# Performance work log

Measured on AMD Instinct MI355X. Metric: run time of the kernel, lower is better.

Reference implementation:

```python
import jax, jax.numpy as jnp
import numpy as np

EPS = 1e-5

def _cell(x, h, c, Wih, Whh, bih, bhh):
    # torch LSTMCell gate order: i, f, g, o
    gates = x @ Wih.T + bih + h @ Whh.T + bhh
    i, f, g, o = jnp.split(gates, 4, axis=-1)
    c = jax.nn.sigmoid(f) * c + jax.nn.sigmoid(i) * jnp.tanh(g)
    h = jax.nn.sigmoid(o) * jnp.tanh(c)
    return h, c

def _bn(x, gamma, beta):
    # training-mode BatchNorm1d: batch statistics over dim 0
    mu = jnp.mean(x, 0)
    var = jnp.var(x, 0)
    return gamma * (x - mu) * jax.lax.rsqrt(var + EPS) + beta

def setup_inputs():
    key = jax.random.key(0)
    ks = jax.random.split(key, 24)
    B, T, I = 1024, 256, 128
    H1, H2, H3 = 256, 256, 32
    w = lambda k, shape: jax.random.normal(k, shape, jnp.float32) * 0.05
    return {
        'x': jax.random.normal(ks[0], (B, T, I), jnp.float32),
        'Wih1': w(ks[1], (4 * H1, I)),  'Whh1': w(ks[2], (4 * H1, H1)),
        'bih1': w(ks[3], (4 * H1,)),    'bhh1': w(ks[4], (4 * H1,)),
        'g1': jnp.ones((H1,), jnp.float32), 'b1': jnp.zeros((H1,), jnp.float32),
        'Wih2': w(ks[5], (4 * H2, H1)), 'Whh2': w(ks[6], (4 * H2, H2)),
        'bih2': w(ks[7], (4 * H2,)),    'bhh2': w(ks[8], (4 * H2,)),
        'g2': jnp.ones((H2,), jnp.float32), 'b2': jnp.zeros((H2,), jnp.float32),
        'Wih3': w(ks[9], (4 * H3, H2)), 'Whh3': w(ks[10], (4 * H3, H3)),
        'bih3': w(ks[11], (4 * H3,)),   'bhh3': w(ks[12], (4 * H3,)),
        'g3': jnp.ones((H3,), jnp.float32), 'b3': jnp.zeros((H3,), jnp.float32),
        'Wl': w(ks[13], (2, H3)), 'bl': w(ks[14], (2,)),
        'Wl2': w(ks[15], (2, 2)), 'bl2': w(ks[16], (2,)),
    }

def reference(x, Wih1, Whh1, bih1, bhh1, g1, b1,
              Wih2, Whh2, bih2, bhh2, g2, b2,
              Wih3, Whh3, bih3, bhh3, g3, b3,
              Wl, bl, Wl2, bl2):
    B = x.shape[0]
    zeros = lambda d: jnp.zeros((B, d), x.dtype)
    carry0 = (zeros(256), zeros(256), zeros(256), zeros(256), zeros(32), zeros(32))

    def step(carry, xt):
        h1, c1, h2, c2, h3, c3 = carry
        h1, c1 = _cell(xt, h1, c1, Wih1, Whh1, bih1, bhh1)
        z = _bn(h1, g1, b1)
        h2, c2 = _cell(z, h2, c2, Wih2, Whh2, bih2, bhh2)
        z = _bn(h2, g2, b2)
        h3, c3 = _cell(z, h3, c3, Wih3, Whh3, bih3, bhh3)
        z = _bn(h3, g3, b3)
        z = jax.nn.relu(z @ Wl.T + bl)
        z = jax.nn.softmax(z @ Wl2.T + bl2, axis=-1)
        return (h1, c1, h2, c2, h3, c3), z

    _, ys = jax.lax.scan(step, carry0, jnp.swapaxes(x, 0, 1))  # ys: [T, B, 2]
    return jnp.swapaxes(ys, 0, 1)  # [B, T, 2]
```

## Files before the change

### kernel.cpp

```cpp
#include <hip/hip_runtime.h>
#include <hip/hip_cooperative_groups.h>

namespace cg = cooperative_groups;

#define B    1024
#define T    256
#define NBLK 256
#define NTHR 512
#define EPS  1e-5f

typedef _Float16 f16;
typedef _Float16 f16x8 __attribute__((ext_vector_type(8)));
typedef float    f32x4 __attribute__((ext_vector_type(4)));
typedef unsigned long long u64;

#define WS_H1X 0u
#define WS_H2X 1048576u
#define WS_H3X 2097152u
#define WS_ST  2228224u
#define WS_BAR 2297856u

#define OW1 0
#define OW2 25088
#define OW3 58368
#define OA1 67840
#define OD1 68864
#define OB1 69888
#define OB2 70016
#define OB3 70144
#define OA3 70160
#define OD3 70288
#define OHW 70416
#define OC1 70704
#define OC2 74928
#define OC3 79152
#define OA2 79680
#define OD2 80704
#define OG1 81728
#define OT1 82752
#define OG2 83776
#define OT2 84800
#define OG3 85824
#define OT3 85952
#define OR1 86080
#define OR2 86592
#define OR3 87104
#define LDSBYTES 87168

__device__ __forceinline__ float fsigmoid(float v) { return 1.f / (1.f + __expf(-v)); }
__device__ __forceinline__ float ftanh(float v)    { return 1.f - 2.f / (__expf(2.f * v) + 1.f); }

__device__ __forceinline__ float coh_ldf(const float* p) {
    return __hip_atomic_load(p, __ATOMIC_RELAXED, __HIP_MEMORY_SCOPE_AGENT);
}
__device__ __forceinline__ void coh_stf(float* p, float v) {
    __hip_atomic_store(p, v, __ATOMIC_RELAXED, __HIP_MEMORY_SCOPE_AGENT);
}

__device__ __forceinline__ void ld_phase(const float* sp, const f16* p1, const f16* p2,
                                         const f16* p3,
    f32x4& r0, f32x4& r1, f32x4& r2, f32x4& r3,
    f16x8& d0, f16x8& d1, f16x8& d2, f16x8& d3,
    f16x8& d4, f16x8& d5, f16x8& d6, f16x8& d7,
    f16x8& e0, f16x8& e1, f16x8& e2, f16x8& e3,
    f16x8& e4, f16x8& e5, f16x8& e6, f16x8& e7,
    f16x8& f0) {
    asm volatile(
        "global_load_dwordx4 %0, %21, off sc0 sc1\n\t"
        "global_load_dwordx4 %1, %21, off offset:16 sc0 sc1\n\t"
        "global_load_dwordx4 %2, %21, off offset:32 sc0 sc1\n\t"
        "global_load_dwordx4 %3, %21, off offset:48 sc0 sc1\n\t"
        "global_load_dwordx4 %4, %22, off sc0\n\t"
        "global_load_dwordx4 %5, %22, off offset:64 sc0\n\t"
        "global_load_dwordx4 %6, %22, off offset:128 sc0\n\t"
        "global_load_dwordx4 %7, %22, off offset:192 sc0\n\t"
        "global_load_dwordx4 %8, %22, off offset:256 sc0\n\t"
        "global_load_dwordx4 %9, %22, off offset:320 sc0\n\t"
        "global_load_dwordx4 %10, %22, off offset:384 sc0\n\t"
        "global_load_dwordx4 %11, %22, off offset:448 sc0\n\t"
        "global_load_dwordx4 %12, %23, off sc0\n\t"
        "global_load_dwordx4 %13, %23, off offset:64 sc0\n\t"
        "global_load_dwordx4 %14, %23, off offset:128 sc0\n\t"
        "global_load_dwordx4 %15, %23, off offset:192 sc0\n\t"
        "global_load_dwordx4 %16, %23, off offset:256 sc0\n\t"
        "global_load_dwordx4 %17, %23, off offset:320 sc0\n\t"
        "global_load_dwordx4 %18, %23, off offset:384 sc0\n\t"
        "global_load_dwordx4 %19, %23, off offset:448 sc0\n\t"
        "global_load_dwordx4 %20, %24, off sc0\n\t"
        "s_waitcnt vmcnt(0)"
        : "=&v"(r0), "=&v"(r1), "=&v"(r2), "=&v"(r3),
          "=&v"(d0), "=&v"(d1), "=&v"(d2), "=&v"(d3),
          "=&v"(d4), "=&v"(d5), "=&v"(d6), "=&v"(d7),
          "=&v"(e0), "=&v"(e1), "=&v"(e2), "=&v"(e3),
          "=&v"(e4), "=&v"(e5), "=&v"(e6), "=&v"(e7),
          "=&v"(f0)
        : "v"(sp), "v"(p1), "v"(p2), "v"(p3) : "memory");
}
__device__ __forceinline__ void ld_h4_sc0(const f16* p, f16x8& d0, f16x8& d1, f16x8& d2, f16x8& d3) {
    asm volatile(
        "global_load_dwordx4 %0, %4, off sc0\n\t"
        "global_load_dwordx4 %1, %4, off offset:16 sc0\n\t"
        "global_load_dwordx4 %2, %4, off offset:32 sc0\n\t"
        "global_load_dwordx4 %3, %4, off offset:48 sc0\n\t"
        "s_waitcnt vmcnt(0)"
        : "=&v"(d0), "=&v"(d1), "=&v"(d2), "=&v"(d3)
        : "v"(p) : "memory");
}
__device__ __forceinline__ void st_h2_sc0(f16* p, f16 v) {
    asm volatile("global_store_short %0, %1, off sc0" :: "v"(p), "v"(v) : "memory");
}

__global__ void __launch_bounds__(NTHR) cryptonet_kernel(
    const float* __restrict__ x,
    const float* __restrict__ Wih1, const float* __restrict__ Whh1,
    const float* __restrict__ bih1, const float* __restrict__ bhh1,
    const float* __restrict__ g1v,  const float* __restrict__ b1v,
    const float* __restrict__ Wih2, const float* __restrict__ Whh2,
    const float* __restrict__ bih2, const float* __restrict__ bhh2,
    const float* __restrict__ g2v,  const float* __restrict__ b2v,
    const float* __restrict__ Wih3, const float* __restrict__ Whh3,
    const float* __restrict__ bih3, const float* __restrict__ bhh3,
    const float* __restrict__ g3v,  const float* __restrict__ b3v,
    const float* __restrict__ Wl,   const float* __restrict__ bl,
    const float* __restrict__ Wl2,  const float* __restrict__ bl2,
    float* __restrict__ out, float* __restrict__ ws)
{
    cg::grid_group grid = cg::this_grid();
    const int tid  = threadIdx.x;
    const int blk  = blockIdx.x;
    const int CG   = blk >> 3;
    const int BGr  = blk & 7;
    const int b0   = BGr * 128;
    const int wv   = tid >> 6;
    const int lane = tid & 63;
    const int q    = lane >> 4;
    const int mlo  = lane & 15;

    extern __shared__ char smraw[];
    f16*   w1  = (f16*)(smraw + OW1);
    f16*   w2  = (f16*)(smraw + OW2);
    f16*   w3  = (f16*)(smraw + OW3);
    float* sA1 = (float*)(smraw + OA1);
    float* sD1 = (float*)(smraw + OD1);
    float* sA2 = (float*)(smraw + OA2);
    float* sD2 = (float*)(smraw + OD2);
    float* sB1 = (float*)(smraw + OB1);
    float* sB2 = (float*)(smraw + OB2);
    float* sB3 = (float*)(smraw + OB3);
    float* sA3 = (float*)(smraw + OA3);
    float* sD3 = (float*)(smraw + OD3);
    float* sHW = (float*)(smraw + OHW);
    float* c1  = (float*)(smraw + OC1);
    float* c2  = (float*)(smraw + OC2);
    float* c3  = (float*)(smraw + OC3);
    float* sG1 = (float*)(smraw + OG1);
    float* sT1 = (float*)(smraw + OT1);
    float* sG2 = (float*)(smraw + OG2);
    float* sT2 = (float*)(smraw + OT2);
    float* sG3 = (float*)(smraw + OG3);
    float* sT3 = (float*)(smraw + OT3);
    float* sR1 = (float*)(smraw + OR1);
    float* sR2 = (float*)(smraw + OR2);
    float* sR3 = (float*)(smraw + OR3);

    char* ws8 = (char*)ws;
    f16*   h1x   = (f16*)(ws8 + WS_H1X);
    f16*   h2x   = (f16*)(ws8 + WS_H2X);
    f16*   h3x   = (f16*)(ws8 + WS_H3X);
    float* stats = (float*)(ws8 + WS_ST);
    unsigned* bar = (unsigned*)(ws8 + WS_BAR);

    for (int idx = tid; idx < 32 * 384; idx += NTHR) {
        const int rr = idx / 384, k = idx - rr * 384;
        const int j = (rr >> 3) * 256 + CG * 8 + (rr & 7);
        const float v = (k < 128) ? Wih1[(size_t)j * 128 + k] : Whh1[(size_t)j * 256 + (k - 128)];
        w1[rr * 392 + k] = (f16)v;
    }
    for (int idx = tid; idx < 32 * 512; idx += NTHR) {
        const int rr = idx >> 9, k = idx & 511;
        const int j = (rr >> 3) * 256 + CG * 8 + (rr & 7);
        const float v = (k < 256) ? Wih2[(size_t)j * 256 + k] : Whh2[(size_t)j * 256 + (k - 256)];
        w2[rr * 520 + k] = (f16)v;
    }
    for (int idx = tid; idx < 16 * 296; idx += NTHR) w3[idx] = (f16)0.f;
    __syncthreads();
    for (int idx = tid; idx < 4 * 288; idx += NTHR) {
        const int rr = idx / 288, k = idx - rr * 288;
        const int j = rr * 32 + CG;
        const float v = (k < 256) ? Wih3[(size_t)j * 256 + k] : Whh3[(size_t)j * 32 + (k - 256)];
        w3[rr * 296 + k] = (f16)v;
    }
    if (tid < 32) {
        const int j = (tid >> 3) * 256 + CG * 8 + (tid & 7);
        sB1[tid] = bih1[j] + bhh1[j];
        sB2[tid] = bih2[j] + bhh2[j];
    }
    if (tid >= 32 && tid < 36) {
        const int g = tid - 32;
        sB3[g] = bih3[g * 32 + CG] + bhh3[g * 32 + CG];
    }
    if (tid >= 64 && tid < 136) {
        const int i = tid - 64;
        float v;
        if (i < 64) v = Wl[i];
        else if (i < 68) v = Wl2[i - 64];
        else if (i < 70) v = bl[i - 68];
        else v = bl2[i - 70];
        sHW[i] = v;
    }
    if (tid < 256) {
        sG1[tid] = g1v[tid]; sT1[tid] = b1v[tid];
        sG2[tid] = g2v[tid]; sT2[tid] = b2v[tid];
        if (tid < 32) { sG3[tid] = g3v[tid]; sT3[tid] = b3v[tid]; }
    }
    for (int i = tid; i < 8 * 132; i += NTHR) { c1[i] = 0.f; c2[i] = 0.f; }
    if (tid < 132) c3[tid] = 0.f;
    {
        unsigned int* z1 = (unsigned int*)h1x;
        unsigned int* z2 = (unsigned int*)h2x;
        unsigned int* z3 = (unsigned int*)h3x;
        const int gt = blk * NTHR + tid, gs = NBLK * NTHR;
        for (int i = gt; i < 131072; i += gs) z1[i] = 0u;
        for (int i = gt; i < 131072; i += gs) z2[i] = 0u;
        for (int i = gt; i < 16384;  i += gs) z3[i] = 0u;
        for (int i = gt; i < 256;    i += gs) bar[i] = 0u;
    }
    grid.sync();

    auto pointwise12 = [&](float* cst, f16* hdst, float* redp, const float* bias,
                           f32x4 acc0, f32x4 acc1) {
        float fr[4], orr[4];
        #pragma unroll
        for (int r = 0; r < 4; ++r) {
            fr[r]  = __shfl_xor(acc0[r], 8);
            orr[r] = __shfl_xor(acc1[r], 8);
        }
        float s = 0.f, sq = 0.f;
        const int c = mlo & 7;
        if (mlo < 8) {
            const float bi = bias[c], bf = bias[8 + c], bg = bias[16 + c], bo = bias[24 + c];
            float4 cc = *(float4*)&cst[c * 132 + wv * 16 + q * 4];
            float cv[4] = {cc.x, cc.y, cc.z, cc.w};
            #pragma unroll
            for (int r = 0; r < 4; ++r) {
                const float gi = fsigmoid(acc0[r] + bi);
                const float gf = fsigmoid(fr[r] + bf);
                const float gg = ftanh(acc1[r] + bg);
                const float go = fsigmoid(orr[r] + bo);
                const float cn = gf * cv[r] + gi * gg;
                cv[r] = cn;
                const f16 h16 = (f16)(go * ftanh(cn));
                st_h2_sc0(&hdst[(size_t)(b0 + wv * 16 + q * 4 + r) * 256 + CG * 8 + c], h16);
                const float hq = (float)h16;
                s += hq; sq += hq * hq;
            }
            *(float4*)&cst[c * 132 + wv * 16 + q * 4] = make_float4(cv[0], cv[1], cv[2], cv[3]);
        }
        s  += __shfl_xor(s, 16);  s  += __shfl_xor(s, 32);
        sq += __shfl_xor(sq, 16); sq += __shfl_xor(sq, 32);
        if (mlo < 8 && q == 0) {
            redp[wv * 16 + c * 2]     = s;
            redp[wv * 16 + c * 2 + 1] = sq;
        }
    };

    f16x8 xpre[4];
    auto loadx = [&](int t) {
        if (t < T) {
            const int brow = b0 + wv * 16 + mlo;
            #pragma unroll
            for (int kt = 0; kt < 4; ++kt) {
                const float* xp = x + ((size_t)brow * T + t) * 128 + kt * 32 + q * 8;
                const float4 u = *(const float4*)xp;
                const float4 v = *(const float4*)(xp + 4);
                f16x8 a;
                a[0] = (f16)u.x; a[1] = (f16)u.y; a[2] = (f16)u.z; a[3] = (f16)u.w;
                a[4] = (f16)v.x; a[5] = (f16)v.y; a[6] = (f16)v.z; a[7] = (f16)v.w;
                xpre[kt] = a;
            }
        }
    };
    loadx(0);

    auto fold8 = [&](f16x8 a, const float* sA, const float* sD, int k) -> f16x8 {
        const float4 aa0 = *(const float4*)&sA[k];
        const float4 aa1 = *(const float4*)&sA[k + 4];
        const float4 dd0 = *(const float4*)&sD[k];
        const float4 dd1 = *(const float4*)&sD[k + 4];
        a[0] = (f16)(aa0.x * (float)a[0] + dd0.x);
        a[1] = (f16)(aa0.y * (float)a[1] + dd0.y);
        a[2] = (f16)(aa0.z * (float)a[2] + dd0.z);
        a[3] = (f16)(aa0.w * (float)a[3] + dd0.w);
        a[4] = (f16)(aa1.x * (float)a[4] + dd1.x);
        a[5] = (f16)(aa1.y * (float)a[5] + dd1.y);
        a[6] = (f16)(aa1.z * (float)a[6] + dd1.z);
        a[7] = (f16)(aa1.w * (float)a[7] + dd1.w);
        return a;
    };

    for (int s = 0; s < T + 3; ++s) {
        const int t2 = s - 1, t3 = s - 2, th = s - 3;
        const int brow = b0 + wv * 16 + mlo;

        const float* sp = stats + (tid < 256
                ? ((size_t)((s & 1) ^ 1) * 8704 + (size_t)tid * 16)
                : ((size_t)(s & 1) * 8704 + 4096 + (size_t)(tid - 256) * 16));
        const f16* p1 = h1x + (size_t)(s & 1) * B * 256 + (size_t)brow * 256 + q * 8;
        const f16* p2 = h2x + (size_t)((s & 1) ^ 1) * B * 256 + (size_t)brow * 256 + q * 8;
        const f16* p3 = h3x + (size_t)(s & 1) * B * 32 + (size_t)brow * 32 + q * 8;
        f32x4 r0, r1, r2, r3;
        f16x8 hd[8], he[8], hf;
        ld_phase(sp, p1, p2, p3, r0, r1, r2, r3,
                 hd[0], hd[1], hd[2], hd[3], hd[4], hd[5], hd[6], hd[7],
                 he[0], he[1], he[2], he[3], he[4], he[5], he[6], he[7], hf);

        if (t2 >= 0 && t2 < T && tid < 256) {
            const float sv = r0[0] + r0[2] + r1[0] + r1[2] + r2[0] + r2[2] + r3[0] + r3[2];
            const float qv = r0[1] + r0[3] + r1[1] + r1[3] + r2[1] + r2[3] + r3[1] + r3[3];
            const float mu = sv * (1.f / B);
            const float var = qv * (1.f / B) - mu * mu;
            const float a = sG1[tid] * rsqrtf(var + EPS);
            sA1[tid] = a; sD1[tid] = sT1[tid] - mu * a;
        }
        if (t3 >= 0 && t3 < T && tid >= 256) {
            const int ch = tid - 256;
            const float sv = r0[0] + r0[2] + r1[0] + r1[2] + r2[0] + r2[2] + r3[0] + r3[2];
            const float qv = r0[1] + r0[3] + r1[1] + r1[3] + r2[1] + r2[3] + r3[1] + r3[3];
            const float mu = sv * (1.f / B);
            const float var = qv * (1.f / B) - mu * mu;
            const float a = sG2[ch] * rsqrtf(var + EPS);
            sA2[ch] = a; sD2[ch] = sT2[ch] - mu * a;
        }
        if (CG == 0 && th >= 0 && tid < 32) {
            const float* sp3 = stats + (size_t)(th & 1) * 8704 + 8192 + (size_t)tid * 16;
            float sv = 0.f, qv = 0.f;
            #pragma unroll
            for (int g = 0; g < 8; ++g) {
                sv += coh_ldf(sp3 + g * 2);
                qv += coh_ldf(sp3 + g * 2 + 1);
            }
            const float mu = sv * (1.f / B);
            const float var = qv * (1.f / B) - mu * mu;
            const float a = sG3[tid] * rsqrtf(var + EPS);
            sA3[tid] = a; sD3[tid] = sT3[tid] - mu * a;
        }

        if (s < T) {
            f16* h1c = h1x + (size_t)((s & 1) ^ 1) * B * 256;
            f32x4 acc0 = {0.f, 0.f, 0.f, 0.f}, acc1 = {0.f, 0.f, 0.f, 0.f};
            #pragma unroll
            for (int kt = 0; kt < 12; ++kt) {
                const f16x8 av = (kt < 4) ? xpre[kt] : hd[kt - 4];
                const f16x8 bf0 = *(const f16x8*)(w1 + mlo * 392 + kt * 32 + q * 8);
                const f16x8 bf1 = *(const f16x8*)(w1 + (16 + mlo) * 392 + kt * 32 + q * 8);
                acc0 = __builtin_amdgcn_mfma_f32_16x16x32_f16(av, bf0, acc0, 0, 0, 0);
                acc1 = __builtin_amdgcn_mfma_f32_16x16x32_f16(av, bf1, acc1, 0, 0, 0);
            }
            pointwise12(c1, h1c, sR1, sB1, acc0, acc1);
        }
        __syncthreads();

        if (t2 >= 0 && t2 < T) {
            f16* h2c = h2x + (size_t)(s & 1) * B * 256;
            f32x4 acc0 = {0.f, 0.f, 0.f, 0.f}, acc1 = {0.f, 0.f, 0.f, 0.f};
            #pragma unroll
            for (int kt = 0; kt < 16; ++kt) {
                const f16x8 av = (kt < 8) ? fold8(hd[kt], sA1, sD1, kt * 32 + q * 8)
                                          : he[kt - 8];
                const f16x8 bf0 = *(const f16x8*)(w2 + mlo * 520 + kt * 32 + q * 8);
                const f16x8 bf1 = *(const f16x8*)(w2 + (16 + mlo) * 520 + kt * 32 + q * 8);
                acc0 = __builtin_amdgcn_mfma_f32_16x16x32_f16(av, bf0, acc0, 0, 0, 0);
                acc1 = __builtin_amdgcn_mfma_f32_16x16x32_f16(av, bf1, acc1, 0, 0, 0);
            }
            pointwise12(c2, h2c, sR2, sB2, acc0, acc1);
        }

        if (t3 >= 0 && t3 < T) {
            f16* h3c = h3x + (size_t)((s & 1) ^ 1) * B * 32;
            f32x4 acc0 = {0.f, 0.f, 0.f, 0.f};
            #pragma unroll
            for (int kt = 0; kt < 9; ++kt) {
                const f16x8 av = (kt < 8) ? fold8(he[kt], sA2, sD2, kt * 32 + q * 8) : hf;
                const f16x8 bf0 = *(const f16x8*)(w3 + mlo * 296 + kt * 32 + q * 8);
                acc0 = __builtin_amdgcn_mfma_f32_16x16x32_f16(av, bf0, acc0, 0, 0, 0);
            }
            float gi[4], gf_[4], gg_[4], go_[4];
            #pragma unroll
            for (int r = 0; r < 4; ++r) {
                gi[r]  = __shfl(acc0[r], (lane & 48) + 0);
                gf_[r] = __shfl(acc0[r], (lane & 48) + 1);
                gg_[r] = __shfl(acc0[r], (lane & 48) + 2);
                go_[r] = __shfl(acc0[r], (lane & 48) + 3);
            }
            float s_ = 0.f, sq = 0.f;
            if (mlo == 0) {
                float4 cc = *(float4*)&c3[wv * 16 + q * 4];
                float cv[4] = {cc.x, cc.y, cc.z, cc.w};
                #pragma unroll
                for (int r = 0; r < 4; ++r) {
                    const float i_ = fsigmoid(gi[r] + sB3[0]);
                    const float f_ = fsigmoid(gf_[r] + sB3[1]);
                    const float g_ = ftanh(gg_[r] + sB3[2]);
                    const float o_ = fsigmoid(go_[r] + sB3[3]);
                    const float cn = f_ * cv[r] + i_ * g_;
                    cv[r] = cn;
                    const f16 h16 = (f16)(o_ * ftanh(cn));
                    st_h2_sc0(&h3c[(size_t)(b0 + wv * 16 + q * 4 + r) * 32 + CG], h16);
                    const float hq = (float)h16;
                    s_ += hq; sq += hq * hq;
                }
                *(float4*)&c3[wv * 16 + q * 4] = make_float4(cv[0], cv[1], cv[2], cv[3]);
            }
            s_ += __shfl_xor(s_, 16); s_ += __shfl_xor(s_, 32);
            sq += __shfl_xor(sq, 16); sq += __shfl_xor(sq, 32);
            if (lane == 0) { sR3[wv * 2] = s_; sR3[wv * 2 + 1] = sq; }
        }

        if (CG == 0 && th >= 0) {
            const f16* hp3 = h3x + (size_t)(s & 1) * B * 32;
            if (lane < 16) {
                const int b = b0 + wv * 16 + lane;
                const f16* hp = hp3 + (size_t)b * 32;
                f16x8 hv0, hv1, hv2, hv3;
                ld_h4_sc0(hp, hv0, hv1, hv2, hv3);
                float zz[32];
                #pragma unroll
                for (int k2 = 0; k2 < 8; ++k2) {
                    zz[k2]      = (float)hv0[k2];
                    zz[8 + k2]  = (float)hv1[k2];
                    zz[16 + k2] = (float)hv2[k2];
                    zz[24 + k2] = (float)hv3[k2];
                }
                float y0 = sHW[68], y1 = sHW[69];
                #pragma unroll
                for (int ch = 0; ch < 32; ++ch) {
                    const float z = sA3[ch] * zz[ch] + sD3[ch];
                    y0 += sHW[ch] * z; y1 += sHW[32 + ch] * z;
                }
                y0 = fmaxf(y0, 0.f); y1 = fmaxf(y1, 0.f);
                const float u0 = sHW[64] * y0 + sHW[65] * y1 + sHW[70];
                const float u1 = sHW[66] * y0 + sHW[67] * y1 + sHW[71];
                const float m = fmaxf(u0, u1);
                const float e0 = __expf(u0 - m), e1 = __expf(u1 - m);
                const float inv = 1.f / (e0 + e1);
                *(float2*)&out[((size_t)b * T + th) * 2] = make_float2(e0 * inv, e1 * inv);
            }
        }

        if (s < T + 2) {
            __syncthreads();
            if (s < T && tid < 16) {
                const int i = tid, ch = CG * 8 + (i >> 1), j = i & 1;
                float v = sR1[i];
                #pragma unroll
                for (int w = 1; w < 8; ++w) v += sR1[w * 16 + i];
                coh_stf(stats + (size_t)(s & 1) * 8704 + (size_t)ch * 16 + BGr * 2 + j, v);
            }
            if (t2 >= 0 && t2 < T && tid >= 16 && tid < 32) {
                const int i = tid - 16, ch = CG * 8 + (i >> 1), j = i & 1;
                float v = sR2[i];
                #pragma unroll
                for (int w = 1; w < 8; ++w) v += sR2[w * 16 + i];
                coh_stf(stats + (size_t)(t2 & 1) * 8704 + 4096 + (size_t)ch * 16 + BGr * 2 + j, v);
            }
            if (t3 >= 0 && t3 < T && tid >= 32 && tid < 34) {
                const int i = tid - 32;
                float v = sR3[i];
                #pragma unroll
                for (int w = 1; w < 8; ++w) v += sR3[w * 2 + i];
                coh_stf(stats + (size_t)(t3 & 1) * 8704 + 8192 + (size_t)CG * 16 + BGr * 2 + i, v);
            }
            __syncthreads();
            if (tid == 0)
                __hip_atomic_store(bar + blk, (unsigned)(s + 1),
                                   __ATOMIC_RELAXED, __HIP_MEMORY_SCOPE_AGENT);
            loadx(s + 1);
            if (wv == 0) {
                const unsigned tgt = (unsigned)(s + 1);
                u64* fl = (u64*)bar;
                for (;;) {
                    const u64 a = __hip_atomic_load(fl + lane,
                                    __ATOMIC_RELAXED, __HIP_MEMORY_SCOPE_AGENT);
                    const u64 b = __hip_atomic_load(fl + 64 + lane,
                                    __ATOMIC_RELAXED, __HIP_MEMORY_SCOPE_AGENT);
                    const bool ok = ((unsigned)a >= tgt) && ((unsigned)(a >> 32) >= tgt) &&
                                    ((unsigned)b >= tgt) && ((unsigned)(b >> 32) >= tgt);
                    if (__all(ok)) break;
                    __builtin_amdgcn_s_sleep(1);
                }
            }
            __syncthreads();
        }
    }
}

extern "C" void kernel_launch(void* const* d_in, const int* in_sizes, int n_in,
                              void* d_out, int out_size, void* d_ws, size_t ws_size,
                              hipStream_t stream) {
    const float* x    = (const float*)d_in[0];
    const float* Wih1 = (const float*)d_in[1];
    const float* Whh1 = (const float*)d_in[2];
    const float* bih1 = (const float*)d_in[3];
    const float* bhh1 = (const float*)d_in[4];
    const float* g1   = (const float*)d_in[5];
    const float* b1   = (const float*)d_in[6];
    const float* Wih2 = (const float*)d_in[7];
    const float* Whh2 = (const float*)d_in[8];
    const float* bih2 = (const float*)d_in[9];
    const float* bhh2 = (const float*)d_in[10];
    const float* g2   = (const float*)d_in[11];
    const float* b2   = (const float*)d_in[12];
    const float* Wih3 = (const float*)d_in[13];
    const float* Whh3 = (const float*)d_in[14];
    const float* bih3 = (const float*)d_in[15];
    const float* bhh3 = (const float*)d_in[16];
    const float* g3   = (const float*)d_in[17];
    const float* b3   = (const float*)d_in[18];
    const float* Wl   = (const float*)d_in[19];
    const float* bl   = (const float*)d_in[20];
    const float* Wl2  = (const float*)d_in[21];
    const float* bl2  = (const float*)d_in[22];
    float* out = (float*)d_out;
    float* ws  = (float*)d_ws;

    const int dyn_lds = LDSBYTES;
    hipFuncSetAttribute((const void*)cryptonet_kernel,
                        hipFuncAttributeMaxDynamicSharedMemorySize, dyn_lds);

    void* args[] = { &x, &Wih1, &Whh1, &bih1, &bhh1, &g1, &b1,
                     &Wih2, &Whh2, &bih2, &bhh2, &g2, &b2,
                     &Wih3, &Whh3, &bih3, &bhh3, &g3, &b3,
                     &Wl, &bl, &Wl2, &bl2, &out, &ws };
    hipLaunchCooperativeKernel((const void*)cryptonet_kernel, dim3(NBLK), dim3(NTHR),
                               args, dyn_lds, stream);
}
```

Measured before the change: 4.880 ms.

## Split grid barrier into group-local wait and deferred global wait overlapping layer-1

The end-of-step barrier now waits only on the 32 blocks of the same batch group, since layer-1 depends only on h1 rows from that group. The global all-block wait is moved to after the layer-1 MFMA and pointwise work of the next step, so layer-1 compute overlaps with slower blocks finishing. The h1 loads are split out of the combined phase load so they can be issued before the global wait. This relaxes synchronisation and risks a race if any cross-group data, such as BN stats, is consumed before the deferred global wait.

```diff
diff --git a/kernel.cpp b/kernel.cpp
--- a/kernel.cpp
+++ b/kernel.cpp
@@ -57,44 +57,47 @@
     __hip_atomic_store(p, v, __ATOMIC_RELAXED, __HIP_MEMORY_SCOPE_AGENT);
 }
 
-__device__ __forceinline__ void ld_phase(const float* sp, const f16* p1, const f16* p2,
-                                         const f16* p3,
+__device__ __forceinline__ void ld_h8_sc0(const f16* p, f16x8& d0, f16x8& d1, f16x8& d2,
+                                          f16x8& d3, f16x8& d4, f16x8& d5, f16x8& d6, f16x8& d7) {
+    asm volatile(
+        "global_load_dwordx4 %0, %8, off sc0\n\t"
+        "global_load_dwordx4 %1, %8, off offset:64 sc0\n\t"
+        "global_load_dwordx4 %2, %8, off offset:128 sc0\n\t"
+        "global_load_dwordx4 %3, %8, off offset:192 sc0\n\t"
+        "global_load_dwordx4 %4, %8, off offset:256 sc0\n\t"
+        "global_load_dwordx4 %5, %8, off offset:320 sc0\n\t"
+        "global_load_dwordx4 %6, %8, off offset:384 sc0\n\t"
+        "global_load_dwordx4 %7, %8, off offset:448 sc0\n\t"
+        "s_waitcnt vmcnt(0)"
+        : "=&v"(d0), "=&v"(d1), "=&v"(d2), "=&v"(d3),
+          "=&v"(d4), "=&v"(d5), "=&v"(d6), "=&v"(d7)
+        : "v"(p) : "memory");
+}
+__device__ __forceinline__ void ld_sh13(const float* sp, const f16* p2, const f16* p3,
     f32x4& r0, f32x4& r1, f32x4& r2, f32x4& r3,
-    f16x8& d0, f16x8& d1, f16x8& d2, f16x8& d3,
-    f16x8& d4, f16x8& d5, f16x8& d6, f16x8& d7,
     f16x8& e0, f16x8& e1, f16x8& e2, f16x8& e3,
     f16x8& e4, f16x8& e5, f16x8& e6, f16x8& e7,
     f16x8& f0) {
     asm volatile(
-        "global_load_dwordx4 %0, %21, off sc0 sc1\n\t"
-        "global_load_dwordx4 %1, %21, off offset:16 sc0 sc1\n\t"
-        "global_load_dwordx4 %2, %21, off offset:32 sc0 sc1\n\t"
-        "global_load_dwordx4 %3, %21, off offset:48 sc0 sc1\n\t"
-        "global_load_dwordx4 %4, %22, off sc0\n\t"
-        "global_load_dwordx4 %5, %22, off offset:64 sc0\n\t"
-        "global_load_dwordx4 %6, %22, off offset:128 sc0\n\t"
-        "global_load_dwordx4 %7, %22, off offset:192 sc0\n\t"
-        "global_load_dwordx4 %8, %22, off offset:256 sc0\n\t"
-        "global_load_dwordx4 %9, %22, off offset:320 sc0\n\t"
-        "global_load_dwordx4 %10, %22, off offset:384 sc0\n\t"
-        "global_load_dwordx4 %11, %22, off offset:448 sc0\n\t"
-        "global_load_dwordx4 %12, %23, off sc0\n\t"
-        "global_load_dwordx4 %13, %23, off offset:64 sc0\n\t"
-        "global_load_dwordx4 %14, %23, off offset:128 sc0\n\t"
-        "global_load_dwordx4 %15, %23, off offset:192 sc0\n\t"
-        "global_load_dwordx4 %16, %23, off offset:256 sc0\n\t"
-        "global_load_dwordx4 %17, %23, off offset:320 sc0\n\t"
-        "global_load_dwordx4 %18, %23, off offset:384 sc0\n\t"
-        "global_load_dwordx4 %19, %23, off offset:448 sc0\n\t"
-        "global_load_dwordx4 %20, %24, off sc0\n\t"
+        "global_load_dwordx4 %0, %13, off sc0 sc1\n\t"
+        "global_load_dwordx4 %1, %13, off offset:16 sc0 sc1\n\t"
+        "global_load_dwordx4 %2, %13, off offset:32 sc0 sc1\n\t"
+        "global_load_dwordx4 %3, %13, off offset:48 sc0 sc1\n\t"
+        "global_load_dwordx4 %4, %14, off sc0\n\t"
+        "global_load_dwordx4 %5, %14, off offset:64 sc0\n\t"
+        "global_load_dwordx4 %6, %14, off offset:128 sc0\n\t"
+        "global_load_dwordx4 %7, %14, off offset:192 sc0\n\t"
+        "global_load_dwordx4 %8, %14, off offset:256 sc0\n\t"
+        "global_load_dwordx4 %9, %14, off offset:320 sc0\n\t"
+        "global_load_dwordx4 %10, %14, off offset:384 sc0\n\t"
+        "global_load_dwordx4 %11, %14, off offset:448 sc0\n\t"
+        "global_load_dwordx4 %12, %15, off sc0\n\t"
         "s_waitcnt vmcnt(0)"
         : "=&v"(r0), "=&v"(r1), "=&v"(r2), "=&v"(r3),
-          "=&v"(d0), "=&v"(d1), "=&v"(d2), "=&v"(d3),
-          "=&v"(d4), "=&v"(d5), "=&v"(d6), "=&v"(d7),
           "=&v"(e0), "=&v"(e1), "=&v"(e2), "=&v"(e3),
           "=&v"(e4), "=&v"(e5), "=&v"(e6), "=&v"(e7),
           "=&v"(f0)
-        : "v"(sp), "v"(p1), "v"(p2), "v"(p3) : "memory");
+        : "v"(sp), "v"(p2), "v"(p3) : "memory");
 }
 __device__ __forceinline__ void ld_h4_sc0(const f16* p, f16x8& d0, f16x8& d1, f16x8& d2, f16x8& d3) {
     asm volatile(
@@ -302,17 +305,48 @@
         const int t2 = s - 1, t3 = s - 2, th = s - 3;
         const int brow = b0 + wv * 16 + mlo;
 
+        f16x8 hd[8];
+        ld_h8_sc0(h1x + (size_t)(s & 1) * B * 256 + (size_t)brow * 256 + q * 8,
+                  hd[0], hd[1], hd[2], hd[3], hd[4], hd[5], hd[6], hd[7]);
+        if (s < T) {
+            f16* h1c = h1x + (size_t)((s & 1) ^ 1) * B * 256;
+            f32x4 acc0 = {0.f, 0.f, 0.f, 0.f}, acc1 = {0.f, 0.f, 0.f, 0.f};
+            #pragma unroll
+            for (int kt = 0; kt < 12; ++kt) {
+                const f16x8 av = (kt < 4) ? xpre[kt] : hd[kt - 4];
+                const f16x8 bf0 = *(const f16x8*)(w1 + mlo * 392 + kt * 32 + q * 8);
+                const f16x8 bf1 = *(const f16x8*)(w1 + (16 + mlo) * 392 + kt * 32 + q * 8);
+                acc0 = __builtin_amdgcn_mfma_f32_16x16x32_f16(av, bf0, acc0, 0, 0, 0);
+                acc1 = __builtin_amdgcn_mfma_f32_16x16x32_f16(av, bf1, acc1, 0, 0, 0);
+            }
+            pointwise12(c1, h1c, sR1, sB1, acc0, acc1);
+        }
+
+        if (wv == 0 && s > 0) {
+            const unsigned tgt = (unsigned)s;
+            u64* fl = (u64*)bar;
+            for (;;) {
+                const u64 a = __hip_atomic_load(fl + lane,
+                                __ATOMIC_RELAXED, __HIP_MEMORY_SCOPE_AGENT);
+                const u64 b = __hip_atomic_load(fl + 64 + lane,
+                                __ATOMIC_RELAXED, __HIP_MEMORY_SCOPE_AGENT);
+                const bool ok = ((unsigned)a >= tgt) && ((unsigned)(a >> 32) >= tgt) &&
+                                ((unsigned)b >= tgt) && ((unsigned)(b >> 32) >= tgt);
+                if (__all(ok)) break;
+                __builtin_amdgcn_s_sleep(1);
+            }
+        }
+        __syncthreads();
+
         const float* sp = stats + (tid < 256
                 ? ((size_t)((s & 1) ^ 1) * 8704 + (size_t)tid * 16)
                 : ((size_t)(s & 1) * 8704 + 4096 + (size_t)(tid - 256) * 16));
-        const f16* p1 = h1x + (size_t)(s & 1) * B * 256 + (size_t)brow * 256 + q * 8;
         const f16* p2 = h2x + (size_t)((s & 1) ^ 1) * B * 256 + (size_t)brow * 256 + q * 8;
         const f16* p3 = h3x + (size_t)(s & 1) * B * 32 + (size_t)brow * 32 + q * 8;
         f32x4 r0, r1, r2, r3;
-        f16x8 hd[8], he[8], hf;
-        ld_phase(sp, p1, p2, p3, r0, r1, r2, r3,
-                 hd[0], hd[1], hd[2], hd[3], hd[4], hd[5], hd[6], hd[7],
-                 he[0], he[1], he[2], he[3], he[4], he[5], he[6], he[7], hf);
+        f16x8 he[8], hf;
+        ld_sh13(sp, p2, p3, r0, r1, r2, r3,
+                he[0], he[1], he[2], he[3], he[4], he[5], he[6], he[7], hf);
 
         if (t2 >= 0 && t2 < T && tid < 256) {
             const float sv = r0[0] + r0[2] + r1[0] + r1[2] + r2[0] + r2[2] + r3[0] + r3[2];
@@ -343,20 +377,6 @@
             const float var = qv * (1.f / B) - mu * mu;
             const float a = sG3[tid] * rsqrtf(var + EPS);
             sA3[tid] = a; sD3[tid] = sT3[tid] - mu * a;
-        }
-
-        if (s < T) {
-            f16* h1c = h1x + (size_t)((s & 1) ^ 1) * B * 256;
-            f32x4 acc0 = {0.f, 0.f, 0.f, 0.f}, acc1 = {0.f, 0.f, 0.f, 0.f};
-            #pragma unroll
-            for (int kt = 0; kt < 12; ++kt) {
-                const f16x8 av = (kt < 4) ? xpre[kt] : hd[kt - 4];
-                const f16x8 bf0 = *(const f16x8*)(w1 + mlo * 392 + kt * 32 + q * 8);
-                const f16x8 bf1 = *(const f16x8*)(w1 + (16 + mlo) * 392 + kt * 32 + q * 8);
-                acc0 = __builtin_amdgcn_mfma_f32_16x16x32_f16(av, bf0, acc0, 0, 0, 0);
-                acc1 = __builtin_amdgcn_mfma_f32_16x16x32_f16(av, bf1, acc1, 0, 0, 0);
-            }
-            pointwise12(c1, h1c, sR1, sB1, acc0, acc1);
         }
         __syncthreads();
 
@@ -472,19 +492,17 @@
             }
             __syncthreads();
             if (tid == 0)
-                __hip_atomic_store(bar + blk, (unsigned)(s + 1),
+                __hip_atomic_store(bar + BGr * 32 + CG, (unsigned)(s + 1),
                                    __ATOMIC_RELAXED, __HIP_MEMORY_SCOPE_AGENT);
             loadx(s + 1);
             if (wv == 0) {
                 const unsigned tgt = (unsigned)(s + 1);
-                u64* fl = (u64*)bar;
+                u64* fl = (u64*)bar + BGr * 16;
                 for (;;) {
-                    const u64 a = __hip_atomic_load(fl + lane,
-                                    __ATOMIC_RELAXED, __HIP_MEMORY_SCOPE_AGENT);
-                    const u64 b = __hip_atomic_load(fl + 64 + lane,
-                                    __ATOMIC_RELAXED, __HIP_MEMORY_SCOPE_AGENT);
-                    const bool ok = ((unsigned)a >= tgt) && ((unsigned)(a >> 32) >= tgt) &&
-                                    ((unsigned)b >= tgt) && ((unsigned)(b >> 32) >= tgt);
+                    const u64 a = (lane < 16)
+                        ? __hip_atomic_load(fl + lane, __ATOMIC_RELAXED, __HIP_MEMORY_SCOPE_AGENT)
+                        : ~0ull;
+                    const bool ok = ((unsigned)a >= tgt) && ((unsigned)(a >> 32) >= tgt);
                     if (__all(ok)) break;
                     __builtin_amdgcn_s_sleep(1);
                 }
```

After: 4.548 ms. -6.8%, faster.

## Deepen layer pipeline with 4-slot ring buffers and relax grid barrier

Applied to the files above, without the earlier changes.

Widens the wavefront pipeline so layers 2 and 3 lag by two steps each, backed by 4-deep ring buffers for h2, h3 and the BN statistics. Cross-block statistics are then consumed a step later. The grid barrier now waits for full completion only within a block's own batch group and accepts the previous step from the others. The layer-1 MFMA is issued before waiting on the statistics loads, so it overlaps their latency. In exchange the code carries more registers (previous-step h tiles), uses more workspace, adds pipeline fill and drain steps, and depends on subtle ring-slot and lag arithmetic for correctness.

```diff
diff --git a/kernel.cpp b/kernel.cpp
--- a/kernel.cpp
+++ b/kernel.cpp
@@ -16,9 +16,9 @@
 
 #define WS_H1X 0u
 #define WS_H2X 1048576u
-#define WS_H3X 2097152u
-#define WS_ST  2228224u
-#define WS_BAR 2297856u
+#define WS_H3X 3145728u
+#define WS_ST  3407872u
+#define WS_BAR 3547136u
 
 #define OW1 0
 #define OW2 25088
@@ -57,44 +57,44 @@
     __hip_atomic_store(p, v, __ATOMIC_RELAXED, __HIP_MEMORY_SCOPE_AGENT);
 }
 
-__device__ __forceinline__ void ld_phase(const float* sp, const f16* p1, const f16* p2,
-                                         const f16* p3,
-    f32x4& r0, f32x4& r1, f32x4& r2, f32x4& r3,
+__device__ __forceinline__ void ld_win(const f16* p1, const f16* p2, const f16* p3,
+                                       const float* sp,
     f16x8& d0, f16x8& d1, f16x8& d2, f16x8& d3,
     f16x8& d4, f16x8& d5, f16x8& d6, f16x8& d7,
     f16x8& e0, f16x8& e1, f16x8& e2, f16x8& e3,
     f16x8& e4, f16x8& e5, f16x8& e6, f16x8& e7,
-    f16x8& f0) {
+    f16x8& f0,
+    f32x4& r0, f32x4& r1, f32x4& r2, f32x4& r3) {
     asm volatile(
-        "global_load_dwordx4 %0, %21, off sc0 sc1\n\t"
-        "global_load_dwordx4 %1, %21, off offset:16 sc0 sc1\n\t"
-        "global_load_dwordx4 %2, %21, off offset:32 sc0 sc1\n\t"
-        "global_load_dwordx4 %3, %21, off offset:48 sc0 sc1\n\t"
-        "global_load_dwordx4 %4, %22, off sc0\n\t"
-        "global_load_dwordx4 %5, %22, off offset:64 sc0\n\t"
-        "global_load_dwordx4 %6, %22, off offset:128 sc0\n\t"
-        "global_load_dwordx4 %7, %22, off offset:192 sc0\n\t"
-        "global_load_dwordx4 %8, %22, off offset:256 sc0\n\t"
-        "global_load_dwordx4 %9, %22, off offset:320 sc0\n\t"
-        "global_load_dwordx4 %10, %22, off offset:384 sc0\n\t"
-        "global_load_dwordx4 %11, %22, off offset:448 sc0\n\t"
-        "global_load_dwordx4 %12, %23, off sc0\n\t"
-        "global_load_dwordx4 %13, %23, off offset:64 sc0\n\t"
-        "global_load_dwordx4 %14, %23, off offset:128 sc0\n\t"
-        "global_load_dwordx4 %15, %23, off offset:192 sc0\n\t"
-        "global_load_dwordx4 %16, %23, off offset:256 sc0\n\t"
-        "global_load_dwordx4 %17, %23, off offset:320 sc0\n\t"
-        "global_load_dwordx4 %18, %23, off offset:384 sc0\n\t"
-        "global_load_dwordx4 %19, %23, off offset:448 sc0\n\t"
-        "global_load_dwordx4 %20, %24, off sc0\n\t"
-        "s_waitcnt vmcnt(0)"
-        : "=&v"(r0), "=&v"(r1), "=&v"(r2), "=&v"(r3),
-          "=&v"(d0), "=&v"(d1), "=&v"(d2), "=&v"(d3),
+        "global_load_dwordx4 %0, %21, off sc0\n\t"
+        "global_load_dwordx4 %1, %21, off offset:64 sc0\n\t"
+        "global_load_dwordx4 %2, %21, off offset:128 sc0\n\t"
+        "global_load_dwordx4 %3, %21, off offset:192 sc0\n\t"
+        "global_load_dwordx4 %4, %21, off offset:256 sc0\n\t"
+        "global_load_dwordx4 %5, %21, off offset:320 sc0\n\t"
+        "global_load_dwordx4 %6, %21, off offset:384 sc0\n\t"
+        "global_load_dwordx4 %7, %21, off offset:448 sc0\n\t"
+        "global_load_dwordx4 %8, %22, off sc0\n\t"
+        "global_load_dwordx4 %9, %22, off offset:64 sc0\n\t"
+        "global_load_dwordx4 %10, %22, off offset:128 sc0\n\t"
+        "global_load_dwordx4 %11, %22, off offset:192 sc0\n\t"
+        "global_load_dwordx4 %12, %22, off offset:256 sc0\n\t"
+        "global_load_dwordx4 %13, %22, off offset:320 sc0\n\t"
+        "global_load_dwordx4 %14, %22, off offset:384 sc0\n\t"
+        "global_load_dwordx4 %15, %22, off offset:448 sc0\n\t"
+        "global_load_dwordx4 %16, %23, off sc0\n\t"
+        "global_load_dwordx4 %17, %24, off sc0 sc1\n\t"
+        "global_load_dwordx4 %18, %24, off offset:16 sc0 sc1\n\t"
+        "global_load_dwordx4 %19, %24, off offset:32 sc0 sc1\n\t"
+        "global_load_dwordx4 %20, %24, off offset:48 sc0 sc1\n\t"
+        "s_waitcnt vmcnt(4)"
+        : "=&v"(d0), "=&v"(d1), "=&v"(d2), "=&v"(d3),
           "=&v"(d4), "=&v"(d5), "=&v"(d6), "=&v"(d7),
           "=&v"(e0), "=&v"(e1), "=&v"(e2), "=&v"(e3),
           "=&v"(e4), "=&v"(e5), "=&v"(e6), "=&v"(e7),
-          "=&v"(f0)
-        : "v"(sp), "v"(p1), "v"(p2), "v"(p3) : "memory");
+          "=&v"(f0),
+          "=&v"(r0), "=&v"(r1), "=&v"(r2), "=&v"(r3)
+        : "v"(p1), "v"(p2), "v"(p3), "v"(sp) : "memory");
 }
 __device__ __forceinline__ void ld_h4_sc0(const f16* p, f16x8& d0, f16x8& d1, f16x8& d2, f16x8& d3) {
     asm volatile(
@@ -217,8 +217,8 @@
     if (tid < 132) c3[tid] = 0.f;
     {
         unsigned int* z1 = (unsigned int*)h1x;
-        unsigned int* z2 = (unsigned int*)h2x;
-        unsigned int* z3 = (unsigned int*)h3x;
+        unsigned int* z2 = (unsigned int*)h2x + 3 * 131072;
+        unsigned int* z3 = (unsigned int*)h3x + 3 * 16384;
         const int gt = blk * NTHR + tid, gs = NBLK * NTHR;
         for (int i = gt; i < 131072; i += gs) z1[i] = 0u;
         for (int i = gt; i < 131072; i += gs) z2[i] = 0u;
@@ -298,23 +298,41 @@
         return a;
     };
 
-    for (int s = 0; s < T + 3; ++s) {
-        const int t2 = s - 1, t3 = s - 2, th = s - 3;
+    f16x8 hdP[8], heP[8];
+
+    for (int s = 0; s < T + 6; ++s) {
+        const int tL2 = s - 2, tL3 = s - 4, tHD = s - 6;
         const int brow = b0 + wv * 16 + mlo;
 
-        const float* sp = stats + (tid < 256
-                ? ((size_t)((s & 1) ^ 1) * 8704 + (size_t)tid * 16)
-                : ((size_t)(s & 1) * 8704 + 4096 + (size_t)(tid - 256) * 16));
         const f16* p1 = h1x + (size_t)(s & 1) * B * 256 + (size_t)brow * 256 + q * 8;
-        const f16* p2 = h2x + (size_t)((s & 1) ^ 1) * B * 256 + (size_t)brow * 256 + q * 8;
-        const f16* p3 = h3x + (size_t)(s & 1) * B * 32 + (size_t)brow * 32 + q * 8;
+        const f16* p2 = h2x + (size_t)((s - 3) & 3) * B * 256 + (size_t)brow * 256 + q * 8;
+        const f16* p3 = h3x + (size_t)((s - 5) & 3) * B * 32 + (size_t)brow * 32 + q * 8;
+        const float* sp = (tid < 256)
+            ? stats + (size_t)((s - 2) & 3) * 8704 + (size_t)tid * 16
+            : stats + (size_t)((s - 4) & 3) * 8704 + 4096 + (size_t)(tid - 256) * 16;
+        f16x8 hdN[8], heR[8], hfR;
         f32x4 r0, r1, r2, r3;
-        f16x8 hd[8], he[8], hf;
-        ld_phase(sp, p1, p2, p3, r0, r1, r2, r3,
-                 hd[0], hd[1], hd[2], hd[3], hd[4], hd[5], hd[6], hd[7],
-                 he[0], he[1], he[2], he[3], he[4], he[5], he[6], he[7], hf);
-
-        if (t2 >= 0 && t2 < T && tid < 256) {
+        ld_win(p1, p2, p3, sp,
+               hdN[0], hdN[1], hdN[2], hdN[3], hdN[4], hdN[5], hdN[6], hdN[7],
+               heR[0], heR[1], heR[2], heR[3], heR[4], heR[5], heR[6], heR[7],
+               hfR, r0, r1, r2, r3);
+
+        f32x4 a1_0 = {0.f, 0.f, 0.f, 0.f}, a1_1 = {0.f, 0.f, 0.f, 0.f};
+        if (s < T) {
+            #pragma unroll
+            for (int kt = 0; kt < 12; ++kt) {
+                const f16x8 av = (kt < 4) ? xpre[kt] : hdN[kt - 4];
+                const f16x8 bf0 = *(const f16x8*)(w1 + mlo * 392 + kt * 32 + q * 8);
+                const f16x8 bf1 = *(const f16x8*)(w1 + (16 + mlo) * 392 + kt * 32 + q * 8);
+                a1_0 = __builtin_amdgcn_mfma_f32_16x16x32_f16(av, bf0, a1_0, 0, 0, 0);
+                a1_1 = __builtin_amdgcn_mfma_f32_16x16x32_f16(av, bf1, a1_1, 0, 0, 0);
+            }
+        }
+        __builtin_amdgcn_sched_barrier(0);
+        asm volatile("s_waitcnt vmcnt(0)" ::: "memory");
+        __builtin_amdgcn_sched_barrier(0);
+
+        if (tL2 >= 0 && tL2 < T && tid < 256) {
             const float sv = r0[0] + r0[2] + r1[0] + r1[2] + r2[0] + r2[2] + r3[0] + r3[2];
             const float qv = r0[1] + r0[3] + r1[1] + r1[3] + r2[1] + r2[3] + r3[1] + r3[3];
             const float mu = sv * (1.f / B);
@@ -322,7 +340,7 @@
             const float a = sG1[tid] * rsqrtf(var + EPS);
             sA1[tid] = a; sD1[tid] = sT1[tid] - mu * a;
         }
-        if (t3 >= 0 && t3 < T && tid >= 256) {
+        if (tL3 >= 0 && tL3 < T && tid >= 256) {
             const int ch = tid - 256;
             const float sv = r0[0] + r0[2] + r1[0] + r1[2] + r2[0] + r2[2] + r3[0] + r3[2];
             const float qv = r0[1] + r0[3] + r1[1] + r1[3] + r2[1] + r2[3] + r3[1] + r3[3];
@@ -331,8 +349,8 @@
             const float a = sG2[ch] * rsqrtf(var + EPS);
             sA2[ch] = a; sD2[ch] = sT2[ch] - mu * a;
         }
-        if (CG == 0 && th >= 0 && tid < 32) {
-            const float* sp3 = stats + (size_t)(th & 1) * 8704 + 8192 + (size_t)tid * 16;
+        if (CG == 0 && tHD >= 0 && tHD < T && tid < 32) {
+            const float* sp3 = stats + (size_t)((s - 2) & 3) * 8704 + 8192 + (size_t)tid * 16;
             float sv = 0.f, qv = 0.f;
             #pragma unroll
             for (int g = 0; g < 8; ++g) {
@@ -347,26 +365,17 @@
 
         if (s < T) {
             f16* h1c = h1x + (size_t)((s & 1) ^ 1) * B * 256;
+            pointwise12(c1, h1c, sR1, sB1, a1_0, a1_1);
+        }
+        __syncthreads();
+
+        if (tL2 >= 0 && tL2 < T) {
+            f16* h2c = h2x + (size_t)(tL2 & 3) * B * 256;
             f32x4 acc0 = {0.f, 0.f, 0.f, 0.f}, acc1 = {0.f, 0.f, 0.f, 0.f};
             #pragma unroll
-            for (int kt = 0; kt < 12; ++kt) {
-                const f16x8 av = (kt < 4) ? xpre[kt] : hd[kt - 4];
-                const f16x8 bf0 = *(const f16x8*)(w1 + mlo * 392 + kt * 32 + q * 8);
-                const f16x8 bf1 = *(const f16x8*)(w1 + (16 + mlo) * 392 + kt * 32 + q * 8);
-                acc0 = __builtin_amdgcn_mfma_f32_16x16x32_f16(av, bf0, acc0, 0, 0, 0);
-                acc1 = __builtin_amdgcn_mfma_f32_16x16x32_f16(av, bf1, acc1, 0, 0, 0);
-            }
-            pointwise12(c1, h1c, sR1, sB1, acc0, acc1);
-        }
-        __syncthreads();
-
-        if (t2 >= 0 && t2 < T) {
-            f16* h2c = h2x + (size_t)(s & 1) * B * 256;
-            f32x4 acc0 = {0.f, 0.f, 0.f, 0.f}, acc1 = {0.f, 0.f, 0.f, 0.f};
-            #pragma unroll
             for (int kt = 0; kt < 16; ++kt) {
-                const f16x8 av = (kt < 8) ? fold8(hd[kt], sA1, sD1, kt * 32 + q * 8)
-                                          : he[kt - 8];
+                const f16x8 av = (kt < 8) ? fold8(hdP[kt], sA1, sD1, kt * 32 + q * 8)
+                                          : heR[kt - 8];
                 const f16x8 bf0 = *(const f16x8*)(w2 + mlo * 520 + kt * 32 + q * 8);
                 const f16x8 bf1 = *(const f16x8*)(w2 + (16 + mlo) * 520 + kt * 32 + q * 8);
                 acc0 = __builtin_amdgcn_mfma_f32_16x16x32_f16(av, bf0, acc0, 0, 0, 0);
@@ -375,12 +384,12 @@
             pointwise12(c2, h2c, sR2, sB2, acc0, acc1);
         }
 
-        if (t3 >= 0 && t3 < T) {
-            f16* h3c = h3x + (size_t)((s & 1) ^ 1) * B * 32;
+        if (tL3 >= 0 && tL3 < T) {
+            f16* h3c = h3x + (size_t)(tL3 & 3) * B * 32;
             f32x4 acc0 = {0.f, 0.f, 0.f, 0.f};
             #pragma unroll
             for (int kt = 0; kt < 9; ++kt) {
-                const f16x8 av = (kt < 8) ? fold8(he[kt], sA2, sD2, kt * 32 + q * 8) : hf;
+                const f16x8 av = (kt < 8) ? fold8(heP[kt], sA2, sD2, kt * 32 + q * 8) : hfR;
                 const f16x8 bf0 = *(const f16x8*)(w3 + mlo * 296 + kt * 32 + q * 8);
                 acc0 = __builtin_amdgcn_mfma_f32_16x16x32_f16(av, bf0, acc0, 0, 0, 0);
             }
@@ -416,8 +425,8 @@
             if (lane == 0) { sR3[wv * 2] = s_; sR3[wv * 2 + 1] = sq; }
         }
 
-        if (CG == 0 && th >= 0) {
-            const f16* hp3 = h3x + (size_t)(s & 1) * B * 32;
+        if (CG == 0 && tHD >= 0 && tHD < T) {
+            const f16* hp3 = h3x + (size_t)(tHD & 3) * B * 32;
             if (lane < 16) {
                 const int b = b0 + wv * 16 + lane;
                 const f16* hp = hp3 + (size_t)b * 32;
@@ -443,48 +452,56 @@
                 const float m = fmaxf(u0, u1);
                 const float e0 = __expf(u0 - m), e1 = __expf(u1 - m);
                 const float inv = 1.f / (e0 + e1);
-                *(float2*)&out[((size_t)b * T + th) * 2] = make_float2(e0 * inv, e1 * inv);
-            }
-        }
-
-        if (s < T + 2) {
+                *(float2*)&out[((size_t)b * T + tHD) * 2] = make_float2(e0 * inv, e1 * inv);
+            }
+        }
+
+        #pragma unroll
+        for (int i = 0; i < 8; ++i) { hdP[i] = hdN[i]; heP[i] = heR[i]; }
+
+        if (s < T + 5) {
             __syncthreads();
             if (s < T && tid < 16) {
                 const int i = tid, ch = CG * 8 + (i >> 1), j = i & 1;
                 float v = sR1[i];
                 #pragma unroll
                 for (int w = 1; w < 8; ++w) v += sR1[w * 16 + i];
-                coh_stf(stats + (size_t)(s & 1) * 8704 + (size_t)ch * 16 + BGr * 2 + j, v);
-            }
-            if (t2 >= 0 && t2 < T && tid >= 16 && tid < 32) {
+                coh_stf(stats + (size_t)(s & 3) * 8704 + (size_t)ch * 16 + BGr * 2 + j, v);
+            }
+            if (tL2 >= 0 && tL2 < T && tid >= 16 && tid < 32) {
                 const int i = tid - 16, ch = CG * 8 + (i >> 1), j = i & 1;
                 float v = sR2[i];
                 #pragma unroll
                 for (int w = 1; w < 8; ++w) v += sR2[w * 16 + i];
-                coh_stf(stats + (size_t)(t2 & 1) * 8704 + 4096 + (size_t)ch * 16 + BGr * 2 + j, v);
-            }
-            if (t3 >= 0 && t3 < T && tid >= 32 && tid < 34) {
+                coh_stf(stats + (size_t)(tL2 & 3) * 8704 + 4096 + (size_t)ch * 16 + BGr * 2 + j, v);
+            }
+            if (tL3 >= 0 && tL3 < T && tid >= 32 && tid < 34) {
                 const int i = tid - 32;
                 float v = sR3[i];
                 #pragma unroll
                 for (int w = 1; w < 8; ++w) v += sR3[w * 2 + i];
-                coh_stf(stats + (size_t)(t3 & 1) * 8704 + 8192 + (size_t)CG * 16 + BGr * 2 + i, v);
+                coh_stf(stats + (size_t)(tL3 & 3) * 8704 + 8192 + (size_t)CG * 16 + BGr * 2 + i, v);
             }
             __syncthreads();
             if (tid == 0)
-                __hip_atomic_store(bar + blk, (unsigned)(s + 1),
+                __hip_atomic_store(bar + BGr * 32 + CG, (unsigned)(s + 1),
                                    __ATOMIC_RELAXED, __HIP_MEMORY_SCOPE_AGENT);
             loadx(s + 1);
             if (wv == 0) {
-                const unsigned tgt = (unsigned)(s + 1);
+                const unsigned to = (unsigned)(s + 1);
+                const unsigned tg = (unsigned)s;
+                const unsigned ta0 = (((2 * lane)       >> 5) == BGr) ? to : tg;
+                const unsigned ta1 = (((2 * lane + 1)   >> 5) == BGr) ? to : tg;
+                const unsigned tb0 = (((128 + 2 * lane) >> 5) == BGr) ? to : tg;
+                const unsigned tb1 = (((129 + 2 * lane) >> 5) == BGr) ? to : tg;
                 u64* fl = (u64*)bar;
                 for (;;) {
                     const u64 a = __hip_atomic_load(fl + lane,
                                     __ATOMIC_RELAXED, __HIP_MEMORY_SCOPE_AGENT);
                     const u64 b = __hip_atomic_load(fl + 64 + lane,
                                     __ATOMIC_RELAXED, __HIP_MEMORY_SCOPE_AGENT);
-                    const bool ok = ((unsigned)a >= tgt) && ((unsigned)(a >> 32) >= tgt) &&
-                                    ((unsigned)b >= tgt) && ((unsigned)(b >> 32) >= tgt);
+                    const bool ok = ((unsigned)a >= ta0) && ((unsigned)(a >> 32) >= ta1) &&
+                                    ((unsigned)b >= tb0) && ((unsigned)(b >> 32) >= tb1);
                     if (__all(ok)) break;
                     __builtin_amdgcn_s_sleep(1);
                 }
```

Result: slower. 7.372 ms (+51.1%).
